# Performance work log

Measured on AMD Instinct MI355X. Metric: run time of the kernel, lower is better.

## Reference

```python
import jax, jax.numpy as jnp
import numpy as np

H = 64        # hidden_dim
A = 21        # N_ACTIONS
B = 262144    # batch size


def setup_inputs() -> dict:
    key = jax.random.key(0)
    ks = jax.random.split(key, 32)

    def w(k, shape):
        fan_in = shape[0]
        return (jax.random.normal(k, shape, jnp.float32) / np.float32(np.sqrt(fan_in)))

    inp = {
        "x": jax.random.normal(ks[0], (B, 2, 2), jnp.float32),
        "b_act1": jax.random.randint(ks[1], (B,), 0, A),
        "b_act2": jax.random.randint(ks[2], (B,), 0, A),
        # enc: Linear(2,H), ReLU, Linear(H,H), ReLU
        "enc_w1": w(ks[3], (2, H)), "enc_b1": jnp.zeros((H,), jnp.float32),
        "enc_w2": w(ks[4], (H, H)), "enc_b2": jnp.zeros((H,), jnp.float32),
        # q_net: Linear(H,H), ReLU, Linear(H,A)
        "q_w1": w(ks[5], (H, H)), "q_b1": jnp.zeros((H,), jnp.float32),
        "q_w2": w(ks[6], (H, A)), "q_b2": jnp.zeros((A,), jnp.float32),
        # v_net: Linear(H,H), ReLU, Linear(H,1)
        "v_w1": w(ks[7], (H, H)), "v_b1": jnp.zeros((H,), jnp.float32),
        "v_w2": w(ks[8], (H, 1)), "v_b2": jnp.zeros((1,), jnp.float32),
        # lin2: Linear(H+A,H), ReLU, Linear(H,H), ReLU, Linear(H,H)
        "l2_w1": w(ks[9], (H + A, H)), "l2_b1": jnp.zeros((H,), jnp.float32),
        "l2_w2": w(ks[10], (H, H)), "l2_b2": jnp.zeros((H,), jnp.float32),
        "l2_w3": w(ks[11], (H, H)), "l2_b3": jnp.zeros((H,), jnp.float32),
        # lin3, lin4
        "l3_w": w(ks[12], (H, H)), "l3_b": jnp.zeros((H,), jnp.float32),
        "l4_w": w(ks[13], (H, A)), "l4_b": jnp.zeros((A,), jnp.float32),
        # q_prime_net: Linear(H,2H) ELU Linear(2H,H) ELU Linear(H,H) ELU Linear(H,1)
        "qp_w1": w(ks[14], (H, 2 * H)), "qp_b1": jnp.zeros((2 * H,), jnp.float32),
        "qp_w2": w(ks[15], (2 * H, H)), "qp_b2": jnp.zeros((H,), jnp.float32),
        "qp_w3": w(ks[16], (H, H)), "qp_b3": jnp.zeros((H,), jnp.float32),
        "qp_w4": w(ks[17], (H, 1)), "qp_b4": jnp.zeros((1,), jnp.float32),
    }
    return inp


def reference(x, b_act1, b_act2,
              enc_w1, enc_b1, enc_w2, enc_b2,
              q_w1, q_b1, q_w2, q_b2,
              v_w1, v_b1, v_w2, v_b2,
              l2_w1, l2_b1, l2_w2, l2_b2, l2_w3, l2_b3,
              l3_w, l3_b, l4_w, l4_b,
              qp_w1, qp_b1, qp_w2, qp_b2, qp_w3, qp_b3, qp_w4, qp_b4):
    relu = jax.nn.relu
    elu = jax.nn.elu

    def enc(z):
        return relu(relu(z @ enc_w1 + enc_b1) @ enc_w2 + enc_b2)

    def q_net(h):
        return relu(h @ q_w1 + q_b1) @ q_w2 + q_b2

    def lin2(e):  # ends with bare Linear (no final activation)
        h = relu(e @ l2_w1 + l2_b1)
        h = relu(h @ l2_w2 + l2_b2)
        return h @ l2_w3 + l2_b3

    def q_prime(z):
        h = elu(z @ qp_w1 + qp_b1)
        h = elu(h @ qp_w2 + qp_b2)
        h = elu(h @ qp_w3 + qp_b3)
        return h @ qp_w4 + qp_b4

    h1 = enc(x[:, 0, :])  # [B,H]
    h2 = enc(x[:, 1, :])
    q1, q2 = q_net(h1), q_net(h2)              # [B,A]
    key2 = jnp.stack([h1, h2], axis=1)          # [B,2,H]
    vtot = relu((h1 + h2) @ v_w1 + v_b1) @ v_w2 + v_b2  # [B,1]

    def joint(act1, act2):
        oh1 = jax.nn.one_hot(act1, A, dtype=h1.dtype)
        oh2 = jax.nn.one_hot(act2, A, dtype=h2.dtype)
        e = jnp.stack([jnp.concatenate([h1, oh1], axis=-1),
                       jnp.concatenate([h2, oh2], axis=-1)], axis=1)  # [B,2,H+A]
        key1 = lin2(e)                              # [B,2,H]
        q = q_prime(key1.mean(axis=1))              # [B,1]
        return key1, q

    key1, joint_qs = joint(b_act1, b_act2)
    a1_max = jnp.argmax(q1, axis=1)
    a2_max = jnp.argmax(q2, axis=1)
    key1_max, joint_max_qs = joint(a1_max, a2_max)

    def q_jt(k1):
        z = key2 + k1.mean(axis=1, keepdims=True) - k1 / 2  # [B,2,H]
        return relu(z @ l3_w + l3_b) @ l4_w + l4_b           # [B,2,A]

    q_jt_alt = q_jt(key1)
    q_jt_max_alt = q_jt(key1_max)

    return (q1, q2, joint_qs, joint_max_qs, vtot, q_jt_alt, q_jt_max_alt)
```

## Files before the change

kernel.cpp:

```cpp
#include <hip/hip_runtime.h>
#include <hip/hip_bf16.h>


#define B_TOT 262144

typedef __bf16 bf16_t;
typedef __bf16 bf16x4 __attribute__((ext_vector_type(4)));
typedef __bf16 bf16x8 __attribute__((ext_vector_type(8)));
typedef float  f32x2  __attribute__((ext_vector_type(2)));
typedef float  f32x4  __attribute__((ext_vector_type(4)));

#define MFMA16(a, b, c) __builtin_amdgcn_mfma_f32_16x16x32_bf16((a), (b), (c), 0, 0, 0)

enum : int {
  OFF_VW1  = 0,
  OFF_L2W1 = 4096,
  OFF_L2W2 = 8192,
  OFF_L2W3 = 12288,
  OFF_L3W  = 16384,
  OFF_L4W  = 20480,
  OFF_QP1  = 22528,
  OFF_QP2  = 30720,
  OFF_QP3  = 38912,
  WS_ELEMS = 43008
};
#define WS_BYTES (WS_ELEMS * 2)

enum : int {
  O_Q1   = 0,
  O_Q2   = 21 * B_TOT,
  O_JQ   = 42 * B_TOT,
  O_JMQ  = 43 * B_TOT,
  O_VT   = 44 * B_TOT,
  O_QJT  = 45 * B_TOT,
  O_QJTM = 87 * B_TOT
};

struct RDesc { const float* src; int K; int N; int NT; int off; };
struct RPack { RDesc d[9]; };

__global__ void repack_kernel(RPack P, bf16_t* __restrict__ ws) {
  RDesc d = P.d[blockIdx.x];
  int n = (d.K >> 5) * d.NT * 512;
  for (int i = threadIdx.x; i < n; i += blockDim.x) {
    int j  = i & 7;
    int l  = (i >> 3) & 63;
    int t  = i >> 9;
    int nt = t % d.NT;
    int kc = t / d.NT;
    int sk = kc * 32 + 16 * (j >> 2) + 4 * (l >> 4) + (j & 3);
    int sn = nt * 16 + (l & 15);
    float v = (sn < d.N) ? d.src[sk * d.N + sn] : 0.0f;
    ws[d.off + i] = (bf16_t)v;
  }
}

struct Args {
  const float* x; const int* a1; const int* a2;
  const float* ew1; const float* eb1; const float* ew2; const float* eb2;
  const float* qw1; const float* qb1; const float* qw2; const float* qb2;
  const float* vw1; const float* vb1; const float* vw2; const float* vb2;
  const float* l2w1; const float* l2b1; const float* l2w2; const float* l2b2;
  const float* l2w3; const float* l2b3;
  const float* l3w;  const float* l3b;  const float* l4w;  const float* l4b;
  const float* qpw1; const float* qpb1; const float* qpw2; const float* qpb2;
  const float* qpw3; const float* qpb3; const float* qpw4; const float* qpb4;
  float* out; const bf16_t* ws;
};

struct __align__(16) SMem {
  unsigned char scr[16896];
  bf16_t h1b[64 * 68];
  bf16_t h2b[64 * 68];
  float  bias[768];
  int    acts[128];
  int    amax[128];
  float  red[64][2];
  int    redi[64][2];
};

__device__ __forceinline__ float eluf(float x) { return x > 0.f ? x : expm1f(x); }

__device__ __forceinline__ void fcA64ip(float* __restrict__ f,
                                        const float* __restrict__ W,
                                        const float* __restrict__ Bv,
                                        bf16_t* __restrict__ hb, int r, int g) {
  f32x2 acc[8];
  const f32x2* Bv2 = (const f32x2*)(Bv + g * 16);
#pragma unroll
  for (int i = 0; i < 8; i++) acc[i] = Bv2[i];
  const f32x2* fr = (const f32x2*)(f + r * 66);
#pragma unroll 1
  for (int hh = 0; hh < 2; hh++) {
    f32x2 in[16];
#pragma unroll
    for (int i = 0; i < 16; i++) in[i] = fr[16 * hh + i];
#pragma unroll 4
    for (int k2 = 0; k2 < 16; k2++) {
      int k = 32 * hh + 2 * k2;
      const f32x2* wr0 = (const f32x2*)(W + k * 64 + g * 16);
      const f32x2* wr1 = (const f32x2*)(W + (k + 1) * 64 + g * 16);
      f32x2 a0 = {in[k2][0], in[k2][0]};
      f32x2 a1 = {in[k2][1], in[k2][1]};
#pragma unroll
      for (int i = 0; i < 8; i++) acc[i] += a0 * wr0[i];
#pragma unroll
      for (int i = 0; i < 8; i++) acc[i] += a1 * wr1[i];
    }
  }
  __syncthreads();
#pragma unroll
  for (int i = 0; i < 8; i++) {
    float v0 = fmaxf(acc[i][0], 0.f), v1 = fmaxf(acc[i][1], 0.f);
    f32x2 v = {v0, v1};
    *(f32x2*)(f + r * 66 + g * 16 + 2 * i) = v;
    if (hb) {
      hb[r * 68 + g * 16 + 2 * i]     = (bf16_t)v0;
      hb[r * 68 + g * 16 + 2 * i + 1] = (bf16_t)v1;
    }
  }
  __syncthreads();
}

template <int NC>
__device__ __forceinline__ void qn2(const float* __restrict__ fin, const float* __restrict__ W21,
                                    const float* __restrict__ Bv, float* __restrict__ qo,
                                    int r, int colbase, float& bv, int& bi) {
  float acc[NC];
#pragma unroll
  for (int i = 0; i < NC; i++) acc[i] = Bv[colbase + i];
  for (int k2 = 0; k2 < 32; k2++) {
    f32x2 a = *(const f32x2*)(fin + r * 66 + 2 * k2);
    const float* wr0 = W21 + (2 * k2) * 21 + colbase;
    const float* wr1 = W21 + (2 * k2 + 1) * 21 + colbase;
#pragma unroll
    for (int i = 0; i < NC; i++) acc[i] = fmaf(a[0], wr0[i], acc[i]);
#pragma unroll
    for (int i = 0; i < NC; i++) acc[i] = fmaf(a[1], wr1[i], acc[i]);
  }
  bv = -3e38f; bi = 0;
#pragma unroll
  for (int i = 0; i < NC; i++) {
    qo[i] = acc[i];
    if (acc[i] > bv) { bv = acc[i]; bi = colbase + i; }
  }
}

template <bool USEWS, int NT, int KC>
__device__ __forceinline__ f32x4 tileT(const bf16x8* __restrict__ WF,
                                       const float* __restrict__ Wp, int N, int woff,
                                       const bf16x8* __restrict__ bin,
                                       const float* __restrict__ bias, int bbase,
                                       int nt, int l, int c, int u) {
  f32x4 a = *(const f32x4*)(bias + bbase + nt * 16 + 4 * u);
#pragma unroll
  for (int kc = 0; kc < KC; kc++) {
    bf16x8 w;
    if constexpr (USEWS) {
      w = WF[(woff >> 3) + (kc * NT + nt) * 64 + l];
    } else {
      int sn = nt * 16 + c;
      if (sn < N) {
#pragma unroll
        for (int j = 0; j < 8; j++)
          w[j] = (bf16_t)Wp[(kc * 32 + 16 * (j >> 2) + 4 * u + (j & 3)) * N + sn];
      } else {
#pragma unroll
        for (int j = 0; j < 8; j++) w[j] = (bf16_t)0.0f;
      }
    }
    a = MFMA16(w, bin[kc], a);
  }
  return a;
}

template <int MODE>
__device__ __forceinline__ bf16x8 pack2(f32x4 t0, f32x4 t1) {
  bf16x8 r;
#pragma unroll
  for (int j = 0; j < 8; j++) {
    float v = (j >> 2) ? t1[j & 3] : t0[j & 3];
    if constexpr (MODE == 1) v = fmaxf(v, 0.f);
    if constexpr (MODE == 2) v = eluf(v);
    r[j] = (bf16_t)v;
  }
  return r;
}

template <bool USEWS>
__global__ __launch_bounds__(256, 4) void qtran_main(Args A) {
  __shared__ SMem sm;
  const int t = threadIdx.x;
  const int wgbase = blockIdx.x * 64;
  const int r = t & 63;
  const int g = __builtin_amdgcn_readfirstlane(t >> 6);

  float* f0 = (float*)sm.scr;

  if (t < 64) {
    sm.bias[t]        = A.vb1[t];
    sm.bias[64 + t]   = A.l2b1[t];
    sm.bias[128 + t]  = A.l2b2[t];
    sm.bias[192 + t]  = A.l2b3[t];
    sm.bias[384 + t]  = A.qpb2[t];
    sm.bias[448 + t]  = A.qpb3[t];
    sm.bias[512 + t]  = A.l3b[t];
    sm.bias[608 + t]  = A.vw2[t];
    sm.bias[672 + t]  = A.qpw4[t];
    sm.acts[t]        = A.a1[wgbase + t];
    sm.acts[64 + t]   = A.a2[wgbase + t];
  } else if (t < 192) {
    sm.bias[256 + t - 64] = A.qpb1[t - 64];
  } else if (t < 224) {
    int i = t - 192;
    sm.bias[576 + i] = (i < 21) ? A.l4b[i] : 0.0f;
  } else if (t == 224) {
    sm.bias[736] = A.vb2[0];
    sm.bias[737] = A.qpb4[0];
  }

  const int rowg = wgbase + r;
  float4 xv = ((const float4*)A.x)[rowg];
#pragma unroll 1
  for (int s = 0; s < 2; ++s) {
    float xa = s ? xv.z : xv.x;
    float xb = s ? xv.w : xv.y;
#pragma unroll
    for (int cc = 0; cc < 16; cc += 2) {
      int col = g * 16 + cc;
      float h0 = fmaf(xa, A.ew1[col],     fmaf(xb, A.ew1[64 + col],     A.eb1[col]));
      float h1 = fmaf(xa, A.ew1[col + 1], fmaf(xb, A.ew1[64 + col + 1], A.eb1[col + 1]));
      f32x2 v = {fmaxf(h0, 0.f), fmaxf(h1, 0.f)};
      *(f32x2*)(f0 + r * 66 + col) = v;
    }
    __syncthreads();
    fcA64ip(f0, A.ew2, A.eb2, s ? sm.h2b : sm.h1b, r, g);
    fcA64ip(f0, A.qw1, A.qb1, nullptr, r, g);
    {
      float* qo = A.out + (s ? O_Q2 : O_Q1) + rowg * 21;
      float bv; int bi;
      if (g == 0) {
        qn2<16>(f0, A.qw2, A.qb2, qo, r, 0, bv, bi);
        sm.red[r][0] = bv; sm.redi[r][0] = bi;
      } else if (g == 1) {
        qn2<5>(f0, A.qw2, A.qb2, qo + 16, r, 16, bv, bi);
        sm.red[r][1] = bv; sm.redi[r][1] = bi;
      }
    }
    __syncthreads();
    if (t < 64)
      sm.amax[s * 64 + t] = (sm.red[t][0] >= sm.red[t][1]) ? sm.redi[t][0] : sm.redi[t][1];
    __syncthreads();
  }

  const int l = t & 63;
  const int c = l & 15, u = l >> 4;
  const int rb = g * 16;
  const int row = rb + c;
  float* out = A.out;
  const bf16x8* WF = (const bf16x8*)A.ws;
  const float* bias = sm.bias;
  float* S = (float*)sm.scr;

  auto HG = [&](const bf16_t* __restrict__ HB, int kc) -> bf16x8 {
    const bf16_t* p = HB + row * 68 + kc * 32 + 4 * u;
    bf16x4 lo = *(const bf16x4*)p;
    bf16x4 hi = *(const bf16x4*)(p + 16);
    bf16x8 rr;
#pragma unroll
    for (int d = 0; d < 4; d++) { rr[d] = lo[d]; rr[4 + d] = hi[d]; }
    return rr;
  };

  {
    bf16x8 aS[2];
#pragma unroll
    for (int kc = 0; kc < 2; kc++) {
      bf16x8 a1 = HG(sm.h1b, kc), a2 = HG(sm.h2b, kc);
      bf16x8 s8;
#pragma unroll
      for (int i = 0; i < 8; i++) s8[i] = (bf16_t)((float)a1[i] + (float)a2[i]);
      aS[kc] = s8;
    }
    float pr = 0.f;
#pragma unroll
    for (int nt = 0; nt < 4; nt++) {
      f32x4 tv = tileT<USEWS, 4, 2>(WF, A.vw1, 64, OFF_VW1, aS, bias, 0, nt, l, c, u);
      f32x4 wv = *(const f32x4*)(bias + 608 + nt * 16 + 4 * u);
#pragma unroll
      for (int p = 0; p < 4; p++) pr += fmaxf(tv[p], 0.f) * wv[p];
    }
    pr += __shfl_xor(pr, 16, 64);
    pr += __shfl_xor(pr, 32, 64);
    if (u == 0) out[O_VT + wgbase + row] = pr + bias[736];
  }

  const int* actsrc[2] = {sm.acts, sm.amax};
  bf16x8 k1f[2][2][2];
  f32x4 msum[2][4];

#pragma unroll
  for (int j = 0; j < 2; j++) {
    const bf16_t* HB = j ? sm.h2b : sm.h1b;
    bf16x8 bh[2];
#pragma unroll
    for (int kc = 0; kc < 2; kc++) bh[kc] = HG(HB, kc);
    f32x4 tS[4];
#pragma unroll
    for (int nt = 0; nt < 4; nt++)
      tS[nt] = tileT<USEWS, 4, 2>(WF, A.l2w1, 64, OFF_L2W1, bh, bias, 64, nt, l, c, u);
    bf16x8 b1[2][2];
#pragma unroll
    for (int x = 0; x < 2; x++) {
      const int act = actsrc[x][j * 64 + row];
      const float* ohp = A.l2w1 + (64 + act) * 64 + 4 * u;
      f32x4 tt0 = tS[0] + *(const f32x4*)(ohp);
      f32x4 tt1 = tS[1] + *(const f32x4*)(ohp + 16);
      f32x4 tt2 = tS[2] + *(const f32x4*)(ohp + 32);
      f32x4 tt3 = tS[3] + *(const f32x4*)(ohp + 48);
      b1[x][0] = pack2<1>(tt0, tt1);
      b1[x][1] = pack2<1>(tt2, tt3);
    }
    bf16x8 b2[2][2];
#pragma unroll
    for (int x = 0; x < 2; x++)
#pragma unroll
      for (int f = 0; f < 2; f++) {
        f32x4 t0 = tileT<USEWS, 4, 2>(WF, A.l2w2, 64, OFF_L2W2, b1[x], bias, 128, 2 * f, l, c, u);
        f32x4 t1 = tileT<USEWS, 4, 2>(WF, A.l2w2, 64, OFF_L2W2, b1[x], bias, 128, 2 * f + 1, l, c, u);
        b2[x][f] = pack2<1>(t0, t1);
      }
#pragma unroll
    for (int x = 0; x < 2; x++)
#pragma unroll
      for (int f = 0; f < 2; f++) {
        f32x4 t0 = tileT<USEWS, 4, 2>(WF, A.l2w3, 64, OFF_L2W3, b2[x], bias, 192, 2 * f, l, c, u);
        f32x4 t1 = tileT<USEWS, 4, 2>(WF, A.l2w3, 64, OFF_L2W3, b2[x], bias, 192, 2 * f + 1, l, c, u);
        k1f[x][j][f] = pack2<0>(t0, t1);
        if (j == 0) { msum[x][2 * f] = t0; msum[x][2 * f + 1] = t1; }
        else        { msum[x][2 * f] += t0; msum[x][2 * f + 1] += t1; }
      }
  }

#pragma unroll
  for (int x = 0; x < 2; x++) {
#pragma unroll
    for (int j = 0; j < 2; j++) {
      const bf16_t* HB = j ? sm.h2b : sm.h1b;
      bf16x8 aZ[2];
#pragma unroll
      for (int kc = 0; kc < 2; kc++) {
        bf16x8 h8 = HG(HB, kc);
        bf16x8 kk = k1f[x][1 - j][kc];
#pragma unroll
        for (int i = 0; i < 8; i++)
          aZ[kc][i] = (bf16_t)((float)h8[i] + 0.5f * (float)kk[i]);
      }
      bf16x8 bz[2];
#pragma unroll
      for (int f = 0; f < 2; f++) {
        f32x4 t0 = tileT<USEWS, 4, 2>(WF, A.l3w, 64, OFF_L3W, aZ, bias, 512, 2 * f, l, c, u);
        f32x4 t1 = tileT<USEWS, 4, 2>(WF, A.l3w, 64, OFF_L3W, aZ, bias, 512, 2 * f + 1, l, c, u);
        bz[f] = pack2<1>(t0, t1);
      }
#pragma unroll
      for (int nt = 0; nt < 2; nt++) {
        f32x4 tq = tileT<USEWS, 2, 2>(WF, A.l4w, 21, OFF_L4W, bz, bias, 576, nt, l, c, u);
#pragma unroll
        for (int p = 0; p < 4; p++) {
          int n2 = nt * 16 + 4 * u + p;
          if (n2 < 21) S[row * 43 + j * 21 + n2] = tq[p];
        }
      }
    }
    const int ob = (x ? O_QJTM : O_QJT) + (wgbase + rb) * 42;
    const float* Sx = S + rb * 43;
    for (int i2 = l; i2 < 672; i2 += 64)
      out[ob + i2] = Sx[(i2 / 42) * 43 + (i2 % 42)];
  }

  {
    bf16x8 aM[2][2];
#pragma unroll
    for (int x = 0; x < 2; x++)
#pragma unroll
      for (int kc = 0; kc < 2; kc++) {
        f32x4 m0 = 0.5f * msum[x][2 * kc], m1 = 0.5f * msum[x][2 * kc + 1];
        aM[x][kc] = pack2<0>(m0, m1);
      }
    bf16x8 bq[2][4];
#pragma unroll
    for (int x = 0; x < 2; x++)
#pragma unroll
      for (int f = 0; f < 4; f++) {
        f32x4 t0 = tileT<USEWS, 8, 2>(WF, A.qpw1, 128, OFF_QP1, aM[x], bias, 256, 2 * f, l, c, u);
        f32x4 t1 = tileT<USEWS, 8, 2>(WF, A.qpw1, 128, OFF_QP1, aM[x], bias, 256, 2 * f + 1, l, c, u);
        bq[x][f] = pack2<2>(t0, t1);
      }
    bf16x8 b3[2][2];
#pragma unroll
    for (int x = 0; x < 2; x++)
#pragma unroll
      for (int f = 0; f < 2; f++) {
        f32x4 t0 = tileT<USEWS, 4, 4>(WF, A.qpw2, 64, OFF_QP2, bq[x], bias, 384, 2 * f, l, c, u);
        f32x4 t1 = tileT<USEWS, 4, 4>(WF, A.qpw2, 64, OFF_QP2, bq[x], bias, 384, 2 * f + 1, l, c, u);
        b3[x][f] = pack2<2>(t0, t1);
      }
    float pj[2] = {0.f, 0.f};
#pragma unroll
    for (int x = 0; x < 2; x++)
#pragma unroll
      for (int nt = 0; nt < 4; nt++) {
        f32x4 tq = tileT<USEWS, 4, 2>(WF, A.qpw3, 64, OFF_QP3, b3[x], bias, 448, nt, l, c, u);
        f32x4 w4 = *(const f32x4*)(bias + 672 + nt * 16 + 4 * u);
#pragma unroll
        for (int p = 0; p < 4; p++) pj[x] += eluf(tq[p]) * w4[p];
      }
#pragma unroll
    for (int x = 0; x < 2; x++) {
      float v = pj[x];
      v += __shfl_xor(v, 16, 64);
      v += __shfl_xor(v, 32, 64);
      if (u == 0) out[(x ? O_JMQ : O_JQ) + wgbase + row] = v + bias[737];
    }
  }
}

extern "C" void kernel_launch(void* const* d_in, const int* in_sizes, int n_in,
                              void* d_out, int out_size, void* d_ws, size_t ws_size,
                              hipStream_t stream) {
  (void)in_sizes; (void)n_in; (void)out_size;
  Args A;
  A.x    = (const float*)d_in[0];
  A.a1   = (const int*)d_in[1];
  A.a2   = (const int*)d_in[2];
  A.ew1  = (const float*)d_in[3];
  A.eb1  = (const float*)d_in[4];
  A.ew2  = (const float*)d_in[5];
  A.eb2  = (const float*)d_in[6];
  A.qw1  = (const float*)d_in[7];
  A.qb1  = (const float*)d_in[8];
  A.qw2  = (const float*)d_in[9];
  A.qb2  = (const float*)d_in[10];
  A.vw1  = (const float*)d_in[11];
  A.vb1  = (const float*)d_in[12];
  A.vw2  = (const float*)d_in[13];
  A.vb2  = (const float*)d_in[14];
  A.l2w1 = (const float*)d_in[15];
  A.l2b1 = (const float*)d_in[16];
  A.l2w2 = (const float*)d_in[17];
  A.l2b2 = (const float*)d_in[18];
  A.l2w3 = (const float*)d_in[19];
  A.l2b3 = (const float*)d_in[20];
  A.l3w  = (const float*)d_in[21];
  A.l3b  = (const float*)d_in[22];
  A.l4w  = (const float*)d_in[23];
  A.l4b  = (const float*)d_in[24];
  A.qpw1 = (const float*)d_in[25];
  A.qpb1 = (const float*)d_in[26];
  A.qpw2 = (const float*)d_in[27];
  A.qpb2 = (const float*)d_in[28];
  A.qpw3 = (const float*)d_in[29];
  A.qpb3 = (const float*)d_in[30];
  A.qpw4 = (const float*)d_in[31];
  A.qpb4 = (const float*)d_in[32];
  A.out  = (float*)d_out;
  A.ws   = (const bf16_t*)d_ws;

  if (ws_size >= (size_t)WS_BYTES) {
    bf16_t* ws = (bf16_t*)d_ws;
    RPack P;
    P.d[0] = {A.vw1,  64, 64,  4, OFF_VW1};
    P.d[1] = {A.l2w1, 64, 64,  4, OFF_L2W1};
    P.d[2] = {A.l2w2, 64, 64,  4, OFF_L2W2};
    P.d[3] = {A.l2w3, 64, 64,  4, OFF_L2W3};
    P.d[4] = {A.l3w,  64, 64,  4, OFF_L3W};
    P.d[5] = {A.l4w,  64, 21,  2, OFF_L4W};
    P.d[6] = {A.qpw1, 64, 128, 8, OFF_QP1};
    P.d[7] = {A.qpw2, 128, 64, 4, OFF_QP2};
    P.d[8] = {A.qpw3, 64, 64,  4, OFF_QP3};
    hipLaunchKernelGGL(repack_kernel, dim3(9), dim3(256), 0, stream, P, ws);
    hipLaunchKernelGGL(HIP_KERNEL_NAME(qtran_main<true>), dim3(B_TOT / 64), dim3(256), 0,
                       stream, A);
  } else {
    hipLaunchKernelGGL(HIP_KERNEL_NAME(qtran_main<false>), dim3(B_TOT / 64), dim3(256), 0,
                       stream, A);
  }
}
```

Before: 977.8 us.

## Process joint passes sequentially in a lambda and relax launch bounds to two waves

Restructures the joint computation so the two action sets (given actions and argmax actions) are processed one after another through a shared lambda, instead of interleaving both through every layer with doubled register arrays. This cuts live register state (k1f, msum, b1/b2, bq per pass). The first lin2 layer, which does not depend on the action, is now computed twice per j instead of once and reused. Launch bounds also drop from 4 to 2 waves-per-EU minimum, giving the compiler more registers per thread at the risk of lower occupancy.

New measurement: 895.1 us. -8.5%, faster.

```diff
diff --git a/kernel.cpp b/kernel.cpp
--- a/kernel.cpp
+++ b/kernel.cpp
@@ -188,7 +188,7 @@
 }
 
 template <bool USEWS>
-__global__ __launch_bounds__(256, 4) void qtran_main(Args A) {
+__global__ __launch_bounds__(256, 2) void qtran_main(Args A) {
   __shared__ SMem sm;
   const int t = threadIdx.x;
   const int wgbase = blockIdx.x * 64;
@@ -295,55 +295,48 @@
     if (u == 0) out[O_VT + wgbase + row] = pr + bias[736];
   }
 
-  const int* actsrc[2] = {sm.acts, sm.amax};
-  bf16x8 k1f[2][2][2];
-  f32x4 msum[2][4];
-
-#pragma unroll
-  for (int j = 0; j < 2; j++) {
-    const bf16_t* HB = j ? sm.h2b : sm.h1b;
-    bf16x8 bh[2];
-#pragma unroll
-    for (int kc = 0; kc < 2; kc++) bh[kc] = HG(HB, kc);
-    f32x4 tS[4];
-#pragma unroll
-    for (int nt = 0; nt < 4; nt++)
-      tS[nt] = tileT<USEWS, 4, 2>(WF, A.l2w1, 64, OFF_L2W1, bh, bias, 64, nt, l, c, u);
-    bf16x8 b1[2][2];
-#pragma unroll
-    for (int x = 0; x < 2; x++) {
-      const int act = actsrc[x][j * 64 + row];
+  auto J = [&](const int* __restrict__ asrc, int jointBase, int qjtBase) {
+    bf16x8 k1f[2][2];
+    f32x4 msum[4];
+#pragma unroll
+    for (int j = 0; j < 2; j++) {
+      const bf16_t* HB = j ? sm.h2b : sm.h1b;
+      const int act = asrc[j * 64 + row];
+      bf16x8 bh[2];
+#pragma unroll
+      for (int kc = 0; kc < 2; kc++) bh[kc] = HG(HB, kc);
       const float* ohp = A.l2w1 + (64 + act) * 64 + 4 * u;
-      f32x4 tt0 = tS[0] + *(const f32x4*)(ohp);
-      f32x4 tt1 = tS[1] + *(const f32x4*)(ohp + 16);
-      f32x4 tt2 = tS[2] + *(const f32x4*)(ohp + 32);
-      f32x4 tt3 = tS[3] + *(const f32x4*)(ohp + 48);
-      b1[x][0] = pack2<1>(tt0, tt1);
-      b1[x][1] = pack2<1>(tt2, tt3);
-    }
-    bf16x8 b2[2][2];
-#pragma unroll
-    for (int x = 0; x < 2; x++)
+      bf16x8 b1[2];
 #pragma unroll
       for (int f = 0; f < 2; f++) {
-        f32x4 t0 = tileT<USEWS, 4, 2>(WF, A.l2w2, 64, OFF_L2W2, b1[x], bias, 128, 2 * f, l, c, u);
-        f32x4 t1 = tileT<USEWS, 4, 2>(WF, A.l2w2, 64, OFF_L2W2, b1[x], bias, 128, 2 * f + 1, l, c, u);
-        b2[x][f] = pack2<1>(t0, t1);
-      }
-#pragma unroll
-    for (int x = 0; x < 2; x++)
+        f32x4 t0 = tileT<USEWS, 4, 2>(WF, A.l2w1, 64, OFF_L2W1, bh, bias, 64, 2 * f, l, c, u);
+        f32x4 t1 = tileT<USEWS, 4, 2>(WF, A.l2w1, 64, OFF_L2W1, bh, bias, 64, 2 * f + 1, l, c, u);
+        t0 += *(const f32x4*)(ohp + (2 * f) * 16);
+        t1 += *(const f32x4*)(ohp + (2 * f + 1) * 16);
+        b1[f] = pack2<1>(t0, t1);
+      }
+      bf16x8 b2[2];
 #pragma unroll
       for (int f = 0; f < 2; f++) {
-        f32x4 t0 = tileT<USEWS, 4, 2>(WF, A.l2w3, 64, OFF_L2W3, b2[x], bias, 192, 2 * f, l, c, u);
-        f32x4 t1 = tileT<USEWS, 4, 2>(WF, A.l2w3, 64, OFF_L2W3, b2[x], bias, 192, 2 * f + 1, l, c, u);
-        k1f[x][j][f] = pack2<0>(t0, t1);
-        if (j == 0) { msum[x][2 * f] = t0; msum[x][2 * f + 1] = t1; }
-        else        { msum[x][2 * f] += t0; msum[x][2 * f + 1] += t1; }
-      }
-  }
-
-#pragma unroll
-  for (int x = 0; x < 2; x++) {
+        f32x4 t0 = tileT<USEWS, 4, 2>(WF, A.l2w2, 64, OFF_L2W2, b1, bias, 128, 2 * f, l, c, u);
+        f32x4 t1 = tileT<USEWS, 4, 2>(WF, A.l2w2, 64, OFF_L2W2, b1, bias, 128, 2 * f + 1, l, c, u);
+        b2[f] = pack2<1>(t0, t1);
+      }
+#pragma unroll
+      for (int f = 0; f < 2; f++) {
+        f32x4 t0 = tileT<USEWS, 4, 2>(WF, A.l2w3, 64, OFF_L2W3, b2, bias, 192, 2 * f, l, c, u);
+        f32x4 t1 = tileT<USEWS, 4, 2>(WF, A.l2w3, 64, OFF_L2W3, b2, bias, 192, 2 * f + 1, l, c, u);
+        k1f[j][f] = pack2<0>(t0, t1);
+        if (j == 0) { msum[2 * f] = t0; msum[2 * f + 1] = t1; }
+        else        { msum[2 * f] += t0; msum[2 * f + 1] += t1; }
+      }
+    }
+    bf16x8 aM[2];
+#pragma unroll
+    for (int kc = 0; kc < 2; kc++) {
+      f32x4 m0 = 0.5f * msum[2 * kc], m1 = 0.5f * msum[2 * kc + 1];
+      aM[kc] = pack2<0>(m0, m1);
+    }
 #pragma unroll
     for (int j = 0; j < 2; j++) {
       const bf16_t* HB = j ? sm.h2b : sm.h1b;
@@ -351,7 +344,7 @@
 #pragma unroll
       for (int kc = 0; kc < 2; kc++) {
         bf16x8 h8 = HG(HB, kc);
-        bf16x8 kk = k1f[x][1 - j][kc];
+        bf16x8 kk = k1f[1 - j][kc];
 #pragma unroll
         for (int i = 0; i < 8; i++)
           aZ[kc][i] = (bf16_t)((float)h8[i] + 0.5f * (float)kk[i]);
@@ -373,57 +366,41 @@
         }
       }
     }
-    const int ob = (x ? O_QJTM : O_QJT) + (wgbase + rb) * 42;
-    const float* Sx = S + rb * 43;
-    for (int i2 = l; i2 < 672; i2 += 64)
-      out[ob + i2] = Sx[(i2 / 42) * 43 + (i2 % 42)];
-  }
-
-  {
-    bf16x8 aM[2][2];
-#pragma unroll
-    for (int x = 0; x < 2; x++)
-#pragma unroll
-      for (int kc = 0; kc < 2; kc++) {
-        f32x4 m0 = 0.5f * msum[x][2 * kc], m1 = 0.5f * msum[x][2 * kc + 1];
-        aM[x][kc] = pack2<0>(m0, m1);
-      }
-    bf16x8 bq[2][4];
-#pragma unroll
-    for (int x = 0; x < 2; x++)
-#pragma unroll
-      for (int f = 0; f < 4; f++) {
-        f32x4 t0 = tileT<USEWS, 8, 2>(WF, A.qpw1, 128, OFF_QP1, aM[x], bias, 256, 2 * f, l, c, u);
-        f32x4 t1 = tileT<USEWS, 8, 2>(WF, A.qpw1, 128, OFF_QP1, aM[x], bias, 256, 2 * f + 1, l, c, u);
-        bq[x][f] = pack2<2>(t0, t1);
-      }
-    bf16x8 b3[2][2];
-#pragma unroll
-    for (int x = 0; x < 2; x++)
-#pragma unroll
-      for (int f = 0; f < 2; f++) {
-        f32x4 t0 = tileT<USEWS, 4, 4>(WF, A.qpw2, 64, OFF_QP2, bq[x], bias, 384, 2 * f, l, c, u);
-        f32x4 t1 = tileT<USEWS, 4, 4>(WF, A.qpw2, 64, OFF_QP2, bq[x], bias, 384, 2 * f + 1, l, c, u);
-        b3[x][f] = pack2<2>(t0, t1);
-      }
-    float pj[2] = {0.f, 0.f};
-#pragma unroll
-    for (int x = 0; x < 2; x++)
-#pragma unroll
-      for (int nt = 0; nt < 4; nt++) {
-        f32x4 tq = tileT<USEWS, 4, 2>(WF, A.qpw3, 64, OFF_QP3, b3[x], bias, 448, nt, l, c, u);
-        f32x4 w4 = *(const f32x4*)(bias + 672 + nt * 16 + 4 * u);
-#pragma unroll
-        for (int p = 0; p < 4; p++) pj[x] += eluf(tq[p]) * w4[p];
-      }
-#pragma unroll
-    for (int x = 0; x < 2; x++) {
-      float v = pj[x];
-      v += __shfl_xor(v, 16, 64);
-      v += __shfl_xor(v, 32, 64);
-      if (u == 0) out[(x ? O_JMQ : O_JQ) + wgbase + row] = v + bias[737];
-    }
-  }
+    {
+      const int ob = qjtBase + (wgbase + rb) * 42;
+      const float* Sx = S + rb * 43;
+      for (int i2 = l; i2 < 672; i2 += 64)
+        out[ob + i2] = Sx[(i2 / 42) * 43 + (i2 % 42)];
+    }
+    bf16x8 bq[4];
+#pragma unroll
+    for (int f = 0; f < 4; f++) {
+      f32x4 t0 = tileT<USEWS, 8, 2>(WF, A.qpw1, 128, OFF_QP1, aM, bias, 256, 2 * f, l, c, u);
+      f32x4 t1 = tileT<USEWS, 8, 2>(WF, A.qpw1, 128, OFF_QP1, aM, bias, 256, 2 * f + 1, l, c, u);
+      bq[f] = pack2<2>(t0, t1);
+    }
+    bf16x8 b3[2];
+#pragma unroll
+    for (int f = 0; f < 2; f++) {
+      f32x4 t0 = tileT<USEWS, 4, 4>(WF, A.qpw2, 64, OFF_QP2, bq, bias, 384, 2 * f, l, c, u);
+      f32x4 t1 = tileT<USEWS, 4, 4>(WF, A.qpw2, 64, OFF_QP2, bq, bias, 384, 2 * f + 1, l, c, u);
+      b3[f] = pack2<2>(t0, t1);
+    }
+    float pj = 0.f;
+#pragma unroll
+    for (int nt = 0; nt < 4; nt++) {
+      f32x4 tq = tileT<USEWS, 4, 2>(WF, A.qpw3, 64, OFF_QP3, b3, bias, 448, nt, l, c, u);
+      f32x4 w4 = *(const f32x4*)(bias + 672 + nt * 16 + 4 * u);
+#pragma unroll
+      for (int p = 0; p < 4; p++) pj += eluf(tq[p]) * w4[p];
+    }
+    pj += __shfl_xor(pj, 16, 64);
+    pj += __shfl_xor(pj, 32, 64);
+    if (u == 0) out[jointBase + wgbase + row] = pj + bias[737];
+  };
+
+  J(sm.acts, O_JQ, O_QJT);
+  J(sm.amax, O_JMQ, O_QJTM);
 }
 
 extern "C" void kernel_launch(void* const* d_in, const int* in_sizes, int n_in,
```
